# Kernel optimization log

Measured on AMD Instinct MI355X. Metric: run time of the kernel, lower is better.

Reference implementation:

```python
import jax, jax.numpy as jnp
import numpy as np

B, H, W, C, NB = 3, 256, 256, 16, 4
EPS = 1e-3  # keras BatchNormalization default epsilon


def _conv(x, w, b):
    y = jax.lax.conv_general_dilated(x, w, (1, 1), 'SAME',
                                     dimension_numbers=('NHWC', 'HWIO', 'NHWC'))
    return y + b


def _bn(x, g, be, mu, v):
    # inference-mode batch norm with moving statistics
    return (x - mu) * jax.lax.rsqrt(v + EPS) * g + be


def _extract_patches(x, p, s):
    # tf.image.extract_patches(..., padding='SAME') -> (b, oh, ow, p, p, c)
    b, h, w, c = x.shape
    oh, ow = -(-h // s), -(-w // s)
    pth = max((oh - 1) * s + p - h, 0)
    ptw = max((ow - 1) * s + p - w, 0)
    xp = jnp.pad(x, ((0, 0), (pth // 2, pth - pth // 2), (ptw // 2, ptw - ptw // 2), (0, 0)))
    ri = np.arange(oh)[:, None] * s + np.arange(p)[None, :]  # (oh, p)
    ci = np.arange(ow)[:, None] * s + np.arange(p)[None, :]  # (ow, p)
    return xp[:, ri[:, None, :, None], ci[None, :, None, :], :]


def setup_inputs() -> dict:
    key = jax.random.key(0)
    ks = jax.random.split(key, 4)
    mr = jax.random.normal(ks[0], (B, H, W, C), jnp.float32)
    pet = jax.random.normal(ks[1], (B, H, W, C), jnp.float32)
    W1 = jax.random.normal(ks[2], (3, 3, C, C * NB), jnp.float32) * 0.05
    W2 = jax.random.normal(ks[3], (3, 3, C * NB, C * NB), jnp.float32) * 0.05
    z = jnp.zeros((C * NB,), jnp.float32)
    o = jnp.ones((C * NB,), jnp.float32)
    return dict(mr_features=mr, pet_features=pet,
                W1=W1, b1=z, g1=o, be1=z, mu1=z, v1=o,
                W2=W2, b2=z, g2=o, be2=z, mu2=z, v2=o,
                patch=8, stride=4)


def reference(mr_features, pet_features, W1, b1, g1, be1, mu1, v1,
              W2, b2, g2, be2, mu2, v2, patch, stride):
    px = py = int(patch)
    sx = sy = int(stride)
    bsz, h, w, c = mr_features.shape

    # ---- B_Kernel_Function_Generator ----
    x = jax.nn.relu(_bn(_conv(mr_features, W1, b1), g1, be1, mu1, v1))
    x = _bn(_conv(x, W2, b2), g2, be2, mu2, v2)  # last conv_block: no activation
    nb = x.shape[-1] // c
    x = x.reshape(bsz, h, w, c, nb)
    x = jax.nn.softmax(x, axis=-1)
    b_features = jnp.where(x > 1e-5, x, 0.0)  # mask * x

    # ---- Sparse_Kernel_Matrix_Multiplication ----
    bc, bf = c, nb
    Nx, Ny = h // px, w // py
    lx, ly = px // sx, py // sy
    SNx, SNy = Nx * lx, Ny * ly

    bflat = b_features.reshape(bsz, h, w, bc * bf)
    bp = _extract_patches(bflat, px, sx).reshape(bsz, SNx, SNy, px, py, bc, bf)
    pp = _extract_patches(pet_features, px, sx).reshape(bsz, SNx, SNy, px, py, bc, 1)

    dn = jnp.sum(bp, axis=(3, 4), keepdims=True)              # diagonal norm
    kp = jnp.sum(pp * bp, axis=(3, 4), keepdims=True)         # kernel-weighted PET
    dn_safe = jnp.where(dn == 0, 1.0, dn)
    kn = jnp.where(dn == 0, 0.0, kp / dn_safe) * bp           # divide_no_nan
    kpet = jnp.sum(kn, axis=-1)                               # (b,SNx,SNy,px,py,bc)

    # deinterleave stride phases: kernel_pet[:, i::lx, j::ly] stack
    kp6 = kpet.reshape(bsz, Nx, lx, Ny, ly, px, py, c)
    st = kp6.transpose(4, 2, 0, 1, 3, 5, 6, 7).reshape(lx * ly, bsz, Nx, Ny, px, py, c)
    t = st.transpose(1, 2, 3, 4, 5, 6, 0).reshape(bsz, Nx, Ny, px, py, c, lx, ly)
    t = t.transpose(0, 1, 3, 2, 4, 5, 6, 7).reshape(bsz, Nx * px, Ny * py, c, lx, ly)
    t = t.transpose(4, 5, 0, 1, 2, 3)  # (lx, ly, b, H, W, c)

    # align_patches: roll each shifted copy back into registration, then mean
    rev = t.transpose(2, 3, 4, 5, 0, 1).reshape(bsz, h, w, c, lx * ly)
    rev = rev.transpose(4, 0, 1, 2, 3)  # (lx*ly, b, H, W, c)
    rollx = np.arange(-px // 2 + sx // 2, px // 2 + sx // 2, sx)
    rolly = np.arange(-py // 2 + sy // 2, py // 2 + sy // 2, sy)
    acc = jnp.zeros((bsz, h, w, c), rev.dtype)
    for m in range(lx * ly):  # small fixed set (lx*ly = 4)
        acc = acc + jnp.roll(rev[m], (int(rollx[m % lx]), int(rolly[m // lx])), axis=(1, 2))
    return acc / (lx * ly)
```

## Files before the change

kernel.cpp:

```cpp
#include <hip/hip_runtime.h>

#define EPSB 1e-3f

typedef _Float16 half8 __attribute__((ext_vector_type(8)));
typedef _Float16 half4 __attribute__((ext_vector_type(4)));
typedef float f32x4 __attribute__((ext_vector_type(4)));

__global__ __launch_bounds__(256, 4)
void k_prep(const float* __restrict__ W1, const float* __restrict__ W2,
            const float* __restrict__ b1, const float* __restrict__ g1,
            const float* __restrict__ be1, const float* __restrict__ mu1,
            const float* __restrict__ v1,
            const float* __restrict__ b2, const float* __restrict__ g2,
            const float* __restrict__ be2, const float* __restrict__ mu2,
            const float* __restrict__ v2,
            _Float16* __restrict__ W1F, _Float16* __restrict__ W2F,
            float* __restrict__ ST)
{
    int t = blockIdx.x * 256 + threadIdx.x;
    if (t < 5 * 4 * 64 * 8) {
        int k = t & 7, lane = (t >> 3) & 63, snt = t >> 9;
        int s = snt >> 2, ct = snt & 3;
        int quad = lane >> 4, n16 = lane & 15;
        int tap = 2 * s + (quad >> 1);
        int ci  = (quad & 1) * 8 + k;
        int co  = ct * 16 + n16;
        float v = (tap < 9) ? W1[(tap * 16 + ci) * 64 + co] : 0.f;
        W1F[t] = (_Float16)v;
        return;
    }
    t -= 5 * 4 * 64 * 8;
    if (t < 18 * 4 * 64 * 8) {
        int k = t & 7, lane = (t >> 3) & 63, snt = t >> 9;
        int s = snt >> 2, ct = snt & 3;
        int quad = lane >> 4, n16 = lane & 15;
        int tap = s >> 1;
        int ci  = (s & 1) * 32 + quad * 8 + k;
        int co  = ct * 16 + n16;
        W2F[t] = (_Float16)W2[(tap * 64 + ci) * 64 + co];
        return;
    }
    t -= 18 * 4 * 64 * 8;
    if (t < 256) {
        int c = t & 63, sel = t >> 6;
        if (sel == 0)      ST[c]       = g1[c] * rsqrtf(v1[c] + EPSB);
        else if (sel == 1) ST[64 + c]  = (b1[c] - mu1[c]) * (g1[c] * rsqrtf(v1[c] + EPSB)) + be1[c];
        else if (sel == 2) ST[128 + c] = g2[c] * rsqrtf(v2[c] + EPSB);
        else               ST[192 + c] = (b2[c] - mu2[c]) * (g2[c] * rsqrtf(v2[c] + EPSB)) + be2[c];
    }
}

#define CIP1 24
__global__ __launch_bounds__(256, 2)
void k_conv1(const float* __restrict__ mr, const _Float16* __restrict__ W1F,
             const float* __restrict__ ST, _Float16* __restrict__ A)
{
    __shared__ __align__(16) _Float16 sM[4 * 64 * 72];
    const int tid = threadIdx.x;
    const int b  = blockIdx.y;
    const int r0 = (blockIdx.x >> 2) * 4;
    const int q0 = (blockIdx.x & 3) * 64;

    for (int idx = tid; idx < 6 * 66 * 2; idx += 256) {
        int c = idx & 1, pp = idx >> 1;
        int p = pp % 66, dy = pp / 66;
        int rr = r0 + dy - 1, qg = q0 + p - 1;
        half8 h = (half8)(_Float16)0.f;
        if ((unsigned)rr < 256u && (unsigned)qg < 256u) {
            const float* src = mr + ((b * 256 + rr) * 256 + qg) * 16 + c * 8;
            float4 v0 = *(const float4*)src;
            float4 v1 = *(const float4*)(src + 4);
            h = (half8){(_Float16)v0.x, (_Float16)v0.y, (_Float16)v0.z, (_Float16)v0.w,
                        (_Float16)v1.x, (_Float16)v1.y, (_Float16)v1.z, (_Float16)v1.w};
        }
        *(half8*)(&sM[(dy * 66 + p) * CIP1 + c * 8]) = h;
    }
    __syncthreads();

    const int w = tid >> 6, lane = tid & 63;
    const int n16 = lane & 15, quad = lane >> 4;
    const int ci0 = (quad & 1) * 8;
    const _Float16* Wl = W1F + lane * 8;

    f32x4 acc[4][4];
    #pragma unroll
    for (int i = 0; i < 4; ++i)
        #pragma unroll
        for (int j = 0; j < 4; ++j) acc[i][j] = (f32x4){0.f, 0.f, 0.f, 0.f};

    half8 wf[2][4], pf[2][4];
    auto load_s = [&](int s, int buf) {
        int tap  = 2 * s + (quad >> 1);
        int tapc = tap > 8 ? 8 : tap;
        int dy = tapc / 3, dx = tapc % 3;
        #pragma unroll
        for (int ct = 0; ct < 4; ++ct)
            wf[buf][ct] = *(const half8*)(Wl + (s * 4 + ct) * 512);
        #pragma unroll
        for (int qt = 0; qt < 4; ++qt)
            pf[buf][qt] = *(const half8*)&sM[((w + dy) * 66 + qt * 16 + n16 + dx) * CIP1 + ci0];
    };
    load_s(0, 0);
    load_s(1, 1);
    #pragma unroll
    for (int s = 0; s < 5; ++s) {
        const int buf = s & 1;
        #pragma unroll
        for (int qt = 0; qt < 4; ++qt)
            #pragma unroll
            for (int ct = 0; ct < 4; ++ct)
                acc[qt][ct] = __builtin_amdgcn_mfma_f32_16x16x32_f16(wf[buf][ct], pf[buf][qt], acc[qt][ct], 0, 0, 0);
        if (s + 2 < 5) load_s(s + 2, buf);
    }

    half4 hv[4][4];
    #pragma unroll
    for (int ct = 0; ct < 4; ++ct) {
        int co0 = ct * 16 + quad * 4;
        f32x4 sc = *(const f32x4*)&ST[co0];
        f32x4 sh = *(const f32x4*)&ST[64 + co0];
        #pragma unroll
        for (int qt = 0; qt < 4; ++qt) {
            half4 h;
            #pragma unroll
            for (int j = 0; j < 4; ++j)
                h[j] = (_Float16)fmaxf(acc[qt][ct][j] * sc[j] + sh[j], 0.f);
            hv[ct][qt] = h;
        }
    }
    __syncthreads();
    #pragma unroll
    for (int ct = 0; ct < 4; ++ct) {
        int co0 = ct * 16 + quad * 4;
        #pragma unroll
        for (int qt = 0; qt < 4; ++qt) {
            int ql = qt * 16 + n16;
            *(half4*)(&sM[(w * 64 + ql) * 72 + co0]) = hv[ct][qt];
        }
    }
    __syncthreads();

    for (int idx = tid; idx < 2048; idx += 256) {
        int rl2 = idx >> 9, rest = idx & 511;
        int ql = rest >> 3, seg = rest & 7;
        int4 v = *(const int4*)&sM[(rl2 * 64 + ql) * 72 + seg * 8];
        *(int4*)(A + (((b * 256 + r0 + rl2) * 256 + q0 + ql) * 64 + seg * 8)) = v;
    }
}

#define CIP2 72
__global__ __launch_bounds__(256, 4)
void k_conv2(const _Float16* __restrict__ A, const _Float16* __restrict__ W2F,
             const float* __restrict__ ST, const float* __restrict__ pet,
             _Float16* __restrict__ BF, float* __restrict__ S2)
{
    __shared__ __align__(16) _Float16 sM[4 * 66 * 64];
    const int tid = threadIdx.x;
    const int b  = blockIdx.y;
    const int r0 = (blockIdx.x >> 2) * 2;
    const int q0 = (blockIdx.x & 3) * 64;

    for (int idx = tid; idx < 4 * 66 * 8; idx += 256) {
        int c = idx & 7, pp = idx >> 3;
        int p = pp % 66;
        int rr = r0 + (pp / 66) - 1, qg = q0 + p - 1;
        int4 v = {0, 0, 0, 0};
        if ((unsigned)rr < 256u && (unsigned)qg < 256u)
            v = *(const int4*)(A + (((b * 256 + rr) * 256 + qg) * 64 + c * 8));
        *(int4*)(&sM[pp * 64 + ((c ^ (p & 7)) << 3)]) = v;
    }
    __syncthreads();

    const int w = tid >> 6, lane = tid & 63;
    const int row = w >> 1;
    const int qh  = (w & 1) * 32;
    const int n16 = lane & 15, quad = lane >> 4;
    const _Float16* Wl = W2F + lane * 8;

    f32x4 acc[2][4];
    #pragma unroll
    for (int i = 0; i < 2; ++i)
        #pragma unroll
        for (int j = 0; j < 4; ++j) acc[i][j] = (f32x4){0.f, 0.f, 0.f, 0.f};

    half8 wf[3][4], pf[3][2];
    auto load_s = [&](int s, int buf) {
        const int tap = s >> 1;
        const int dy = tap / 3, dx = tap % 3;
        const int slot = (s & 1) * 4 + quad;
        const int sxm = (n16 + dx) & 7;
        #pragma unroll
        for (int ct = 0; ct < 4; ++ct)
            wf[buf][ct] = *(const half8*)(Wl + (s * 4 + ct) * 512);
        #pragma unroll
        for (int qt = 0; qt < 2; ++qt)
            pf[buf][qt] = *(const half8*)&sM[((row + dy) * 66 + qh + qt * 16 + n16 + dx) * 64 + ((slot ^ sxm) << 3)];
    };
    load_s(0, 0);
    load_s(1, 1);
    load_s(2, 2);
    #pragma unroll
    for (int s = 0; s < 18; ++s) {
        const int buf = s % 3;
        #pragma unroll
        for (int qt = 0; qt < 2; ++qt)
            #pragma unroll
            for (int ct = 0; ct < 4; ++ct)
                acc[qt][ct] = __builtin_amdgcn_mfma_f32_16x16x32_f16(wf[buf][ct], pf[buf][qt], acc[qt][ct], 0, 0, 0);
        if (s + 3 < 18) load_s(s + 3, buf);
    }

    half4 hv[4][2];
    #pragma unroll
    for (int ct = 0; ct < 4; ++ct) {
        int co0 = ct * 16 + quad * 4;
        f32x4 sc = *(const f32x4*)&ST[128 + co0];
        f32x4 sh = *(const f32x4*)&ST[192 + co0];
        #pragma unroll
        for (int qt = 0; qt < 2; ++qt) {
            float z0 = acc[qt][ct][0] * sc[0] + sh[0];
            float z1 = acc[qt][ct][1] * sc[1] + sh[1];
            float z2 = acc[qt][ct][2] * sc[2] + sh[2];
            float z3 = acc[qt][ct][3] * sc[3] + sh[3];
            float mx = fmaxf(fmaxf(z0, z1), fmaxf(z2, z3));
            float e0 = __expf(z0 - mx), e1 = __expf(z1 - mx);
            float e2 = __expf(z2 - mx), e3 = __expf(z3 - mx);
            float inv = __builtin_amdgcn_rcpf((e0 + e1) + (e2 + e3));
            float p0 = e0 * inv, p1 = e1 * inv, p2 = e2 * inv, p3 = e3 * inv;
            half4 h;
            h[0] = (_Float16)(p0 > 1e-5f ? p0 : 0.f);
            h[1] = (_Float16)(p1 > 1e-5f ? p1 : 0.f);
            h[2] = (_Float16)(p2 > 1e-5f ? p2 : 0.f);
            h[3] = (_Float16)(p3 > 1e-5f ? p3 : 0.f);
            hv[ct][qt] = h;
        }
    }
    __syncthreads();
    #pragma unroll
    for (int ct = 0; ct < 4; ++ct) {
        int co0 = ct * 16 + quad * 4;
        #pragma unroll
        for (int qt = 0; qt < 2; ++qt) {
            int ql = qh + qt * 16 + n16;
            *(half4*)(&sM[(row * 64 + ql) * CIP2 + co0]) = hv[ct][qt];
        }
    }
    __syncthreads();

    for (int idx = tid; idx < 1024; idx += 256) {
        int rl2 = idx >> 9, rest = idx & 511;
        int ql = rest >> 3, seg = rest & 7;
        int4 v = *(const int4*)&sM[(rl2 * 64 + ql) * CIP2 + seg * 8];
        *(int4*)(BF + (((b * 256 + r0 + rl2) * 256 + q0 + ql) * 64 + seg * 8)) = v;
    }

    const int qp = tid >> 3, chg = tid & 7;
    {
        float dn[8], kp[8];
        #pragma unroll
        for (int j = 0; j < 8; ++j) { dn[j] = 0.f; kp[j] = 0.f; }
        #pragma unroll
        for (int u = 0; u < 2; ++u)
            #pragma unroll
            for (int v = 0; v < 2; ++v) {
                int rl = u, ql = 2 * qp + v;
                half8 bf = *(const half8*)(&sM[(rl * 64 + ql) * CIP2 + chg * 8]);
                float2 p2 = *(const float2*)(pet + ((b * 256 + r0 + rl) * 256 + q0 + ql) * 16 + chg * 2);
                #pragma unroll
                for (int j = 0; j < 8; ++j) {
                    float bv = (float)bf[j];
                    dn[j] += bv;
                    kp[j] = fmaf((j < 4) ? p2.x : p2.y, bv, kp[j]);
                }
            }
        float* o = S2 + 2 * ((size_t)(((b * 128 + (r0 >> 1)) * 128 + (q0 >> 1) + qp) * 64) + chg * 8);
        #pragma unroll
        for (int m = 0; m < 4; ++m)
            *(float4*)(o + 4 * m) = make_float4(dn[2*m], kp[2*m], dn[2*m+1], kp[2*m+1]);
    }
}

__global__ __launch_bounds__(256, 4)
void k_ratio(const float* __restrict__ S2, float* __restrict__ RATIO)
{
    int t = blockIdx.x * 256 + threadIdx.x;
    int cf = t & 63;
    int j  = (t >> 6) & 63;
    int i  = (t >> 12) & 63;
    int b  = t >> 18;
    float dn = 0.f, kp = 0.f;
    #pragma unroll
    for (int u = 0; u < 4; ++u) {
        int r2 = 2 * i - 1 + u;
        if ((unsigned)r2 >= 128u) continue;
        #pragma unroll
        for (int v = 0; v < 4; ++v) {
            int q2 = 2 * j - 1 + v;
            if ((unsigned)q2 >= 128u) continue;
            float2 s = *(const float2*)(S2 + 2 * (((b * 128 + r2) * 128 + q2) * 64 + cf));
            dn += s.x;
            kp += s.y;
        }
    }
    RATIO[t] = (dn == 0.f) ? 0.f : 0.25f * kp * __builtin_amdgcn_rcpf(dn);
}

__global__ __launch_bounds__(256, 4)
void k_out(const _Float16* __restrict__ BF, const float* __restrict__ RATIO,
           float* __restrict__ out)
{
    __shared__ __align__(16) float sU[64 * 68];
    const int tid = threadIdx.x;
    const int r = blockIdx.x & 255;
    const int b = blockIdx.x >> 8;

    const int i0 = (r <= 253) ? 2 * ((r + 2) >> 3)       : -1;
    const int i1 = (r >= 2)   ? 2 * ((r - 2) >> 3) + 1   : -1;

    for (int idx = tid; idx < 1024; idx += 256) {
        int j = idx >> 4, c4 = idx & 15;
        float4 a = make_float4(0.f, 0.f, 0.f, 0.f);
        if (i0 >= 0) a = *(const float4*)&RATIO[(((b * 64 + i0) * 64 + j) << 6) + 4 * c4];
        float4 bb = make_float4(0.f, 0.f, 0.f, 0.f);
        if (i1 >= 0) bb = *(const float4*)&RATIO[(((b * 64 + i1) * 64 + j) << 6) + 4 * c4];
        *(float4*)&sU[j * 68 + 4 * c4] = make_float4(a.x + bb.x, a.y + bb.y, a.z + bb.z, a.w + bb.w);
    }
    __syncthreads();

    const int q = tid;
    const int j0 = (q <= 253) ? 2 * ((q + 2) >> 3)     : -1;
    const int j1 = (q >= 2)   ? 2 * ((q - 2) >> 3) + 1 : -1;

    const half8* bfp = (const half8*)(BF + ((size_t)(b * 256 + r) * 256 + q) * 64);
    float o[16];
    #pragma unroll
    for (int c = 0; c < 16; ++c) o[c] = 0.f;

    #pragma unroll
    for (int c2 = 0; c2 < 8; ++c2) {
        half8 bf8 = bfp[c2];
        float s0 = 0.f, s1 = 0.f;
        #pragma unroll
        for (int pj = 0; pj < 2; ++pj) {
            int jj = pj ? j1 : j0;
            if (jj < 0) continue;
            const float* up = &sU[jj * 68 + 8 * c2];
            s0 += (float)bf8[0] * up[0] + (float)bf8[1] * up[1]
                + (float)bf8[2] * up[2] + (float)bf8[3] * up[3];
            s1 += (float)bf8[4] * up[4] + (float)bf8[5] * up[5]
                + (float)bf8[6] * up[6] + (float)bf8[7] * up[7];
        }
        o[2 * c2]     = s0;
        o[2 * c2 + 1] = s1;
    }
    float* op = out + ((size_t)(b * 256 + r) * 256 + q) * 16;
    #pragma unroll
    for (int m = 0; m < 4; ++m)
        *(float4*)(op + 4 * m) = make_float4(o[4*m], o[4*m+1], o[4*m+2], o[4*m+3]);
}

extern "C" void kernel_launch(void* const* d_in, const int* in_sizes, int n_in,
                              void* d_out, int out_size, void* d_ws, size_t ws_size,
                              hipStream_t stream) {
    const float* mr  = (const float*)d_in[0];
    const float* pet = (const float*)d_in[1];
    const float* W1  = (const float*)d_in[2];
    const float* b1  = (const float*)d_in[3];
    const float* g1  = (const float*)d_in[4];
    const float* be1 = (const float*)d_in[5];
    const float* mu1 = (const float*)d_in[6];
    const float* v1  = (const float*)d_in[7];
    const float* W2  = (const float*)d_in[8];
    const float* b2  = (const float*)d_in[9];
    const float* g2  = (const float*)d_in[10];
    const float* be2 = (const float*)d_in[11];
    const float* mu2 = (const float*)d_in[12];
    const float* v2  = (const float*)d_in[13];

    char* ws = (char*)d_ws;
    _Float16* A     = (_Float16*)(ws);
    _Float16* BF    = (_Float16*)(ws + 25165824);
    float*    S2    = (float*)(ws + 50331648);
    float*    RATIO = (float*)(ws + 75497472);
    _Float16* W1F   = (_Float16*)(ws + 78643200);
    _Float16* W2F   = (_Float16*)(ws + 78663680);
    float*    ST    = (float*)(ws + 78737408);
    float*    out   = (float*)d_out;

    dim3 blk(256);
    k_prep<<<185, blk, 0, stream>>>(W1, W2, b1, g1, be1, mu1, v1,
                                    b2, g2, be2, mu2, v2, W1F, W2F, ST);
    k_conv1<<<dim3(256, 3), blk, 0, stream>>>(mr, W1F, ST, A);
    k_conv2<<<dim3(512, 3), blk, 0, stream>>>(A, W2F, ST, pet, BF, S2);
    k_ratio<<<3072, blk, 0, stream>>>(S2, RATIO);
    k_out<<<768, blk, 0, stream>>>(BF, RATIO, out);
}
```

Measured before the change: 170.7 us.

## Fuse conv1 into conv2 kernel with halo recompute in shared memory

Merges the first convolution into the second convolution kernel. Each block computes the conv1 output tile plus its one-pixel halo (4x66) straight into shared memory from an mr tile with a two-pixel halo, so the 64-channel fp16 intermediate is never written to or read back from global memory. The cost is recomputing the halo rows and columns of conv1 in every block, plus more shared memory per block with occupancy lowered to 3 blocks per CU. One kernel launch is also removed.

```diff
diff --git a/kernel.cpp b/kernel.cpp
--- a/kernel.cpp
+++ b/kernel.cpp
@@ -50,21 +50,25 @@
     }
 }
 
-#define CIP1 24
-__global__ __launch_bounds__(256, 2)
-void k_conv1(const float* __restrict__ mr, const _Float16* __restrict__ W1F,
-             const float* __restrict__ ST, _Float16* __restrict__ A)
+#define CIPM 20
+#define CIP2 72
+__global__ __launch_bounds__(256, 3)
+void k_convf(const float* __restrict__ mr, const _Float16* __restrict__ W1F,
+             const _Float16* __restrict__ W2F, const float* __restrict__ ST,
+             const float* __restrict__ pet,
+             _Float16* __restrict__ BF, float* __restrict__ S2)
 {
-    __shared__ __align__(16) _Float16 sM[4 * 64 * 72];
+    __shared__ __align__(16) _Float16 sMR[6 * 68 * CIPM];
+    __shared__ __align__(16) _Float16 sC1[4 * 66 * 64];
     const int tid = threadIdx.x;
     const int b  = blockIdx.y;
-    const int r0 = (blockIdx.x >> 2) * 4;
+    const int r0 = (blockIdx.x >> 2) * 2;
     const int q0 = (blockIdx.x & 3) * 64;
 
-    for (int idx = tid; idx < 6 * 66 * 2; idx += 256) {
+    for (int idx = tid; idx < 6 * 68 * 2; idx += 256) {
         int c = idx & 1, pp = idx >> 1;
-        int p = pp % 66, dy = pp / 66;
-        int rr = r0 + dy - 1, qg = q0 + p - 1;
+        int p = pp % 68, dys = pp / 68;
+        int rr = r0 + dys - 2, qg = q0 + p - 2;
         half8 h = (half8)(_Float16)0.f;
         if ((unsigned)rr < 256u && (unsigned)qg < 256u) {
             const float* src = mr + ((b * 256 + rr) * 256 + qg) * 16 + c * 8;
@@ -73,108 +77,69 @@
             h = (half8){(_Float16)v0.x, (_Float16)v0.y, (_Float16)v0.z, (_Float16)v0.w,
                         (_Float16)v1.x, (_Float16)v1.y, (_Float16)v1.z, (_Float16)v1.w};
         }
-        *(half8*)(&sM[(dy * 66 + p) * CIP1 + c * 8]) = h;
+        *(half8*)(&sMR[pp * CIPM + c * 8]) = h;
     }
     __syncthreads();
 
     const int w = tid >> 6, lane = tid & 63;
     const int n16 = lane & 15, quad = lane >> 4;
-    const int ci0 = (quad & 1) * 8;
-    const _Float16* Wl = W1F + lane * 8;
-
-    f32x4 acc[4][4];
-    #pragma unroll
-    for (int i = 0; i < 4; ++i)
-        #pragma unroll
-        for (int j = 0; j < 4; ++j) acc[i][j] = (f32x4){0.f, 0.f, 0.f, 0.f};
-
-    half8 wf[2][4], pf[2][4];
-    auto load_s = [&](int s, int buf) {
-        int tap  = 2 * s + (quad >> 1);
-        int tapc = tap > 8 ? 8 : tap;
-        int dy = tapc / 3, dx = tapc % 3;
-        #pragma unroll
-        for (int ct = 0; ct < 4; ++ct)
-            wf[buf][ct] = *(const half8*)(Wl + (s * 4 + ct) * 512);
-        #pragma unroll
-        for (int qt = 0; qt < 4; ++qt)
-            pf[buf][qt] = *(const half8*)&sM[((w + dy) * 66 + qt * 16 + n16 + dx) * CIP1 + ci0];
-    };
-    load_s(0, 0);
-    load_s(1, 1);
-    #pragma unroll
-    for (int s = 0; s < 5; ++s) {
-        const int buf = s & 1;
-        #pragma unroll
-        for (int qt = 0; qt < 4; ++qt)
-            #pragma unroll
-            for (int ct = 0; ct < 4; ++ct)
-                acc[qt][ct] = __builtin_amdgcn_mfma_f32_16x16x32_f16(wf[buf][ct], pf[buf][qt], acc[qt][ct], 0, 0, 0);
-        if (s + 2 < 5) load_s(s + 2, buf);
-    }
-
-    half4 hv[4][4];
-    #pragma unroll
-    for (int ct = 0; ct < 4; ++ct) {
-        int co0 = ct * 16 + quad * 4;
-        f32x4 sc = *(const f32x4*)&ST[co0];
-        f32x4 sh = *(const f32x4*)&ST[64 + co0];
-        #pragma unroll
-        for (int qt = 0; qt < 4; ++qt) {
-            half4 h;
-            #pragma unroll
-            for (int j = 0; j < 4; ++j)
-                h[j] = (_Float16)fmaxf(acc[qt][ct][j] * sc[j] + sh[j], 0.f);
-            hv[ct][qt] = h;
-        }
-    }
-    __syncthreads();
-    #pragma unroll
-    for (int ct = 0; ct < 4; ++ct) {
-        int co0 = ct * 16 + quad * 4;
-        #pragma unroll
-        for (int qt = 0; qt < 4; ++qt) {
-            int ql = qt * 16 + n16;
-            *(half4*)(&sM[(w * 64 + ql) * 72 + co0]) = hv[ct][qt];
-        }
-    }
-    __syncthreads();
-
-    for (int idx = tid; idx < 2048; idx += 256) {
-        int rl2 = idx >> 9, rest = idx & 511;
-        int ql = rest >> 3, seg = rest & 7;
-        int4 v = *(const int4*)&sM[(rl2 * 64 + ql) * 72 + seg * 8];
-        *(int4*)(A + (((b * 256 + r0 + rl2) * 256 + q0 + ql) * 64 + seg * 8)) = v;
-    }
-}
-
-#define CIP2 72
-__global__ __launch_bounds__(256, 4)
-void k_conv2(const _Float16* __restrict__ A, const _Float16* __restrict__ W2F,
-             const float* __restrict__ ST, const float* __restrict__ pet,
-             _Float16* __restrict__ BF, float* __restrict__ S2)
-{
-    __shared__ __align__(16) _Float16 sM[4 * 66 * 64];
-    const int tid = threadIdx.x;
-    const int b  = blockIdx.y;
-    const int r0 = (blockIdx.x >> 2) * 2;
-    const int q0 = (blockIdx.x & 3) * 64;
-
-    for (int idx = tid; idx < 4 * 66 * 8; idx += 256) {
-        int c = idx & 7, pp = idx >> 3;
-        int p = pp % 66;
-        int rr = r0 + (pp / 66) - 1, qg = q0 + p - 1;
-        int4 v = {0, 0, 0, 0};
-        if ((unsigned)rr < 256u && (unsigned)qg < 256u)
-            v = *(const int4*)(A + (((b * 256 + rr) * 256 + qg) * 64 + c * 8));
-        *(int4*)(&sM[pp * 64 + ((c ^ (p & 7)) << 3)]) = v;
-    }
-    __syncthreads();
-
-    const int w = tid >> 6, lane = tid & 63;
+
+    {
+        const _Float16* Wl1 = W1F + lane * 8;
+        const int ci0 = (quad & 1) * 8;
+        #pragma unroll
+        for (int k = 0; k < 5; ++k) {
+            const int g  = w + 4 * k;
+            const int y  = g / 5;
+            const int xi = g % 5;
+            const int x0 = xi * 13 - ((xi >> 2) << 1);
+            const int px = x0 + n16;
+
+            f32x4 a1[4];
+            #pragma unroll
+            for (int ct = 0; ct < 4; ++ct) a1[ct] = (f32x4){0.f, 0.f, 0.f, 0.f};
+
+            half8 wf1[2][4], pf1[2];
+            auto load1 = [&](int s, int buf) {
+                int tap  = 2 * s + (quad >> 1);
+                int tapc = tap > 8 ? 8 : tap;
+                int dy = tapc / 3, dx = tapc % 3;
+                #pragma unroll
+                for (int ct = 0; ct < 4; ++ct)
+                    wf1[buf][ct] = *(const half8*)(Wl1 + (s * 4 + ct) * 512);
+                pf1[buf] = *(const half8*)&sMR[((y + dy) * 68 + px + dx) * CIPM + ci0];
+            };
+            load1(0, 0);
+            load1(1, 1);
+            #pragma unroll
+            for (int s = 0; s < 5; ++s) {
+                const int buf = s & 1;
+                #pragma unroll
+                for (int ct = 0; ct < 4; ++ct)
+                    a1[ct] = __builtin_amdgcn_mfma_f32_16x16x32_f16(wf1[buf][ct], pf1[buf], a1[ct], 0, 0, 0);
+                if (s + 2 < 5) load1(s + 2, buf);
+            }
+
+            const bool valid = ((unsigned)(r0 - 1 + y) < 256u) && ((unsigned)(q0 - 1 + px) < 256u);
+            #pragma unroll
+            for (int ct = 0; ct < 4; ++ct) {
+                int co0 = ct * 16 + quad * 4;
+                f32x4 sc = *(const f32x4*)&ST[co0];
+                f32x4 sh = *(const f32x4*)&ST[64 + co0];
+                half4 h;
+                #pragma unroll
+                for (int j = 0; j < 4; ++j)
+                    h[j] = (_Float16)fmaxf(a1[ct][j] * sc[j] + sh[j], 0.f);
+                if (!valid) h = (half4)(_Float16)0.f;
+                int slot = ct * 2 + (quad >> 1);
+                *(half4*)&sC1[(y * 66 + px) * 64 + ((slot ^ (px & 7)) << 3) + (quad & 1) * 4] = h;
+            }
+        }
+    }
+    __syncthreads();
+
     const int row = w >> 1;
     const int qh  = (w & 1) * 32;
-    const int n16 = lane & 15, quad = lane >> 4;
     const _Float16* Wl = W2F + lane * 8;
 
     f32x4 acc[2][4];
@@ -194,7 +159,7 @@
             wf[buf][ct] = *(const half8*)(Wl + (s * 4 + ct) * 512);
         #pragma unroll
         for (int qt = 0; qt < 2; ++qt)
-            pf[buf][qt] = *(const half8*)&sM[((row + dy) * 66 + qh + qt * 16 + n16 + dx) * 64 + ((slot ^ sxm) << 3)];
+            pf[buf][qt] = *(const half8*)&sC1[((row + dy) * 66 + qh + qt * 16 + n16 + dx) * 64 + ((slot ^ sxm) << 3)];
     };
     load_s(0, 0);
     load_s(1, 1);
@@ -242,7 +207,7 @@
         #pragma unroll
         for (int qt = 0; qt < 2; ++qt) {
             int ql = qh + qt * 16 + n16;
-            *(half4*)(&sM[(row * 64 + ql) * CIP2 + co0]) = hv[ct][qt];
+            *(half4*)(&sC1[(row * 64 + ql) * CIP2 + co0]) = hv[ct][qt];
         }
     }
     __syncthreads();
@@ -250,7 +215,7 @@
     for (int idx = tid; idx < 1024; idx += 256) {
         int rl2 = idx >> 9, rest = idx & 511;
         int ql = rest >> 3, seg = rest & 7;
-        int4 v = *(const int4*)&sM[(rl2 * 64 + ql) * CIP2 + seg * 8];
+        int4 v = *(const int4*)&sC1[(rl2 * 64 + ql) * CIP2 + seg * 8];
         *(int4*)(BF + (((b * 256 + r0 + rl2) * 256 + q0 + ql) * 64 + seg * 8)) = v;
     }
 
@@ -264,7 +229,7 @@
             #pragma unroll
             for (int v = 0; v < 2; ++v) {
                 int rl = u, ql = 2 * qp + v;
-                half8 bf = *(const half8*)(&sM[(rl * 64 + ql) * CIP2 + chg * 8]);
+                half8 bf = *(const half8*)(&sC1[(rl * 64 + ql) * CIP2 + chg * 8]);
                 float2 p2 = *(const float2*)(pet + ((b * 256 + r0 + rl) * 256 + q0 + ql) * 16 + chg * 2);
                 #pragma unroll
                 for (int j = 0; j < 8; ++j) {
@@ -378,20 +343,18 @@
     const float* v2  = (const float*)d_in[13];
 
     char* ws = (char*)d_ws;
-    _Float16* A     = (_Float16*)(ws);
-    _Float16* BF    = (_Float16*)(ws + 25165824);
-    float*    S2    = (float*)(ws + 50331648);
-    float*    RATIO = (float*)(ws + 75497472);
-    _Float16* W1F   = (_Float16*)(ws + 78643200);
-    _Float16* W2F   = (_Float16*)(ws + 78663680);
-    float*    ST    = (float*)(ws + 78737408);
+    _Float16* BF    = (_Float16*)(ws);
+    float*    S2    = (float*)(ws + 25165824);
+    float*    RATIO = (float*)(ws + 50331648);
+    _Float16* W1F   = (_Float16*)(ws + 53477376);
+    _Float16* W2F   = (_Float16*)(ws + 53497856);
+    float*    ST    = (float*)(ws + 53571584);
     float*    out   = (float*)d_out;
 
     dim3 blk(256);
     k_prep<<<185, blk, 0, stream>>>(W1, W2, b1, g1, be1, mu1, v1,
                                     b2, g2, be2, mu2, v2, W1F, W2F, ST);
-    k_conv1<<<dim3(256, 3), blk, 0, stream>>>(mr, W1F, ST, A);
-    k_conv2<<<dim3(512, 3), blk, 0, stream>>>(A, W2F, ST, pet, BF, S2);
+    k_convf<<<dim3(512, 3), blk, 0, stream>>>(mr, W1F, W2F, ST, pet, BF, S2);
     k_ratio<<<3072, blk, 0, stream>>>(S2, RATIO);
     k_out<<<768, blk, 0, stream>>>(BF, RATIO, out);
 }
```

After: 170.4 us. No clear change (-0.1%).
